# Kernel tuning notes

Hardware: AMD Instinct MI355X
Metric: run time of the kernel (lower is better)

## Reference

```python
import jax, jax.numpy as jnp
import numpy as np
from jax import lax
from jax.scipy.ndimage import map_coordinates

L = 10  # unrolled iterations (LayerNo)


def _conv(x, w, b):
    # x [N,C,H,W], w [O,I,3,3] -> 'SAME' padding == padding=1 for k=3
    y = lax.conv_general_dilated(x, w, (1, 1), 'SAME',
                                 dimension_numbers=('NCHW', 'OIHW', 'NCHW'))
    return y + b[None, :, None, None]


def _prelu(x, a):
    return jnp.where(x >= 0, x, a * x)


def _block(x, w1, b1, a1, w2, b2, a2, w3, b3):
    x = _prelu(_conv(x, w1, b1), a1)
    x = _prelu(_conv(x, w2, b2), a2)
    return _conv(x, w3, b3)


def _radon_forward(img, theta, det_count):
    # img [S,S]; parallel-beam line integrals -> [A, det_count]
    S = img.shape[0]
    c = (S - 1) / 2.0
    s = jnp.arange(det_count, dtype=img.dtype) - (det_count - 1) / 2.0
    t = jnp.arange(S, dtype=img.dtype) - (S - 1) / 2.0

    def one(a):
        ca, sa = jnp.cos(a), jnp.sin(a)
        x = s[:, None] * ca - t[None, :] * sa  # [D,S] sample cols
        y = s[:, None] * sa + t[None, :] * ca  # [D,S] sample rows
        vals = map_coordinates(img, [y + c, x + c], order=1, mode='constant', cval=0.0)
        return vals.sum(axis=1)

    return jax.vmap(one)(theta)


def _radon_backprojection(sino, theta, S):
    # sino [A,D] -> [S,S] (adjoint smear with bilinear detector interpolation)
    A, D = sino.shape
    c = (S - 1) / 2.0
    dc = (D - 1) / 2.0
    ax = jnp.arange(S, dtype=sino.dtype) - c
    Y, X = jnp.meshgrid(ax, ax, indexing='ij')  # row=y, col=x

    def one(row, a):
        ca, sa = jnp.cos(a), jnp.sin(a)
        sidx = (X * ca + Y * sa + dc).ravel()
        return map_coordinates(row, [sidx], order=1, mode='constant', cval=0.0).reshape(S, S)

    return jax.vmap(one)(sino, theta).sum(axis=0)


def _filter_sinogram(sino):
    # Ram-Lak ramp filter along detector axis with FBP normalization pi/(2*A)
    A, D = sino.shape
    n = 2048  # next power of two >= 2*D (D=729)
    F = jnp.fft.rfft(sino, n=n, axis=-1)
    ramp = (2.0 * jnp.fft.rfftfreq(n)).astype(sino.dtype)
    out = jnp.fft.irfft(F * ramp, n=n, axis=-1)[..., :D]
    return out * (jnp.pi / (2.0 * A))


def _forward(cond, x0, g, theta, theta_label,
             dw1, db1, da1, dw2, db2, da2, dw3, db3,
             pw1, pb1, pa1, pw2, pb2, pa2, pw3, pb3):
    S = x0.shape[2]
    A, D = g.shape[2], g.shape[3]
    h = jnp.zeros((1, 5, A, D), dtype=g.dtype)
    f = jnp.zeros((1, 5, S, S), dtype=g.dtype)
    for i in range(L):
        Op_f = _radon_forward(f[0, 1], theta, D)[None, None]          # [1,1,A,D]
        h = h + _block(jnp.concatenate([h, Op_f, g], axis=1),
                       dw1[i], db1[i], da1[i], dw2[i], db2[i], da2[i], dw3[i], db3[i])
        h1 = _filter_sinogram(h[0, 0])                                 # [A,D]
        OpAdj_h = _radon_backprojection(h1, theta, S)[None, None]      # [1,1,S,S]
        f = f + _block(jnp.concatenate([f, OpAdj_h], axis=1),
                       pw1[i], pb1[i], pa1[i], pw2[i], pb2[i], pa2[i], pw3[i], pb3[i])
    return (f[:, 0:1], f[:, 0:1], f[:, 0:1])


def setup_inputs() -> dict:
    key = jax.random.key(0)
    ks = jax.random.split(key, 12)
    S, A, D = 512, 60, 729

    def xavier(k, shp):
        cout, cin = shp[1], shp[2]
        std = np.sqrt(2.0 / ((cin + cout) * 9.0)).astype(np.float32)
        return jax.random.normal(k, shp, dtype=jnp.float32) * std

    ang = jnp.linspace(0.0, np.pi, A, endpoint=False).astype(jnp.float32)
    return {
        'cond': jax.random.normal(ks[0], (1, 1, S, S), dtype=jnp.float32),
        'x0': jax.random.normal(ks[1], (1, 1, S, S), dtype=jnp.float32),
        'g': jax.random.normal(ks[2], (1, 1, A, D), dtype=jnp.float32),
        'theta': ang,
        'theta_label': ang,
        'dw1': xavier(ks[3], (L, 32, 7, 3, 3)), 'db1': jnp.zeros((L, 32), jnp.float32), 'da1': 0.25 * jnp.ones((L,), jnp.float32),
        'dw2': xavier(ks[4], (L, 32, 32, 3, 3)), 'db2': jnp.zeros((L, 32), jnp.float32), 'da2': 0.25 * jnp.ones((L,), jnp.float32),
        'dw3': xavier(ks[5], (L, 5, 32, 3, 3)), 'db3': jnp.zeros((L, 5), jnp.float32),
        'pw1': xavier(ks[6], (L, 32, 6, 3, 3)), 'pb1': jnp.zeros((L, 32), jnp.float32), 'pa1': 0.25 * jnp.ones((L,), jnp.float32),
        'pw2': xavier(ks[7], (L, 32, 32, 3, 3)), 'pb2': jnp.zeros((L, 32), jnp.float32), 'pa2': 0.25 * jnp.ones((L,), jnp.float32),
        'pw3': xavier(ks[8], (L, 5, 32, 3, 3)), 'pb3': jnp.zeros((L, 5), jnp.float32),
    }


def reference(cond, x0, g, theta, theta_label,
              dw1, db1, da1, dw2, db2, da2, dw3, db3,
              pw1, pb1, pa1, pw2, pb2, pa2, pw3, pb3):
    return _forward(cond, x0, g, theta, theta_label,
                    dw1, db1, da1, dw2, db2, da2, dw3, db3,
                    pw1, pb1, pa1, pw2, pb2, pa2, pw3, pb3)
```

## Files before the change

kernel.cpp:

```cpp
#include <hip/hip_runtime.h>
#include <math.h>

#define SS 512
#define AANG 60
#define DDET 729
#define NPIX (SS*SS)
#define NSIN (AANG*DDET)
#define NTAPS 1457
#define DRS 768

typedef float v4u __attribute__((ext_vector_type(4), aligned(4)));
typedef float v4a __attribute__((ext_vector_type(4), aligned(16)));
typedef float v2u __attribute__((ext_vector_type(2), aligned(8)));
typedef float v2a __attribute__((ext_vector_type(2), aligned(4)));
typedef short short8 __attribute__((ext_vector_type(8)));
typedef short short4v __attribute__((ext_vector_type(4)));
typedef float f32x4 __attribute__((ext_vector_type(4)));

__device__ inline unsigned short f2bf(float x){
  unsigned u = __float_as_uint(x);
  return (unsigned short)((u + 0x7fffu + ((u >> 16) & 1u)) >> 16);
}

__global__ void trig_kernel(const float* __restrict__ theta, float* __restrict__ trig){
  int a = threadIdx.x;
  if (a < AANG){ trig[a] = cosf(theta[a]); trig[AANG+a] = sinf(theta[a]); }
}

__global__ void taps_kernel(float* __restrict__ taps){
  __shared__ double red[256];
  int m  = blockIdx.x;
  int mm = m - 728;
  double s = 0.0;
  for (int k = 1 + (int)threadIdx.x; k <= 1023; k += 256){
    int phase = (k*mm) & 2047;
    s += (double)k * cos((double)phase * (M_PI/1024.0));
  }
  red[threadIdx.x] = s;
  __syncthreads();
  for (int off=128; off; off>>=1){
    if ((int)threadIdx.x < off) red[threadIdx.x] += red[threadIdx.x+off];
    __syncthreads();
  }
  if (threadIdx.x==0){
    double x = (red[0]*(1.0/512.0) + ((mm & 1) ? -1.0 : 1.0)) / 2048.0;
    taps[m] = (float)(x * (M_PI/120.0));
  }
}

__global__ void transpose_all(const float* __restrict__ s2, float* __restrict__ d2,
                              const float* __restrict__ s5, float* __restrict__ d5){
  int idx = blockIdx.x*256 + (int)threadIdx.x;
  const float* src; float* dst;
  int Cout = 5, Cin = 32;
  if      (idx < 14400){              src=s2; dst=d2; }
  else if (idx < 28800){ idx-=14400;  src=s5; dst=d5; }
  else return;
  int t = idx % 9; int r = idx/9;
  int i = r % Cin; r /= Cin;
  int o = r % Cout; int l = r/Cout;
  dst[((l*Cin+i)*9+t)*Cout+o] = src[idx];
}

__global__ void transpose_w8(const float* __restrict__ src, float* __restrict__ dst, int Cin){
  int idx = blockIdx.x*256 + (int)threadIdx.x;
  int tot = 10*32*Cin*9;
  if (idx >= tot) return;
  int t = idx % 9; int r = idx/9;
  int i = r % Cin; r /= Cin;
  int o = r % 32; int l = r/32;
  int cg = o >> 3, u = o & 7;
  dst[(((l*Cin + i)*4 + cg)*9 + t)*8 + u] = src[idx];
}

__global__ void prep_bimg(const float* __restrict__ w, unsigned short* __restrict__ B){
  int idx = blockIdx.x*256 + (int)threadIdx.x;
  if (idx >= 10*9*2*64*8) return;
  int j    =  idx        & 7;
  int lane = (idx >> 3)  & 63;
  int n    = (idx >> 9)  & 1;
  int r    =  idx >> 10;
  int tap = r % 9, l = r / 9;
  int c = (lane >> 4)*8 + j;
  int o = n*16 + (lane & 15);
  float x = w[(((size_t)(l*32+o)*32 + c)*9) + tap];
  unsigned short hb = f2bf(x);
  float hf = __uint_as_float((unsigned)hb << 16);
  unsigned short lb = f2bf(x - hf);
  size_t d = (size_t)l*18432 + (size_t)tap*2048 + n*1024 + lane*8 + j;
  B[d]       = hb;
  B[d + 512] = lb;
}

__global__ void prep_bimg3(const float* __restrict__ w, unsigned short* __restrict__ B){
  int idx = blockIdx.x*256 + (int)threadIdx.x;
  if (idx >= 10*9*64*8) return;
  int j    =  idx       & 7;
  int lane = (idx >> 3) & 63;
  int r    =  idx >> 9;
  int tap = r % 9, l = r / 9;
  int c = (lane >> 4)*8 + j;
  int o = lane & 15;
  float x = (o < 5) ? w[(((size_t)(l*5+o)*32 + c)*9) + tap] : 0.f;
  unsigned short hb = f2bf(x);
  float hf = __uint_as_float((unsigned)hb << 16);
  unsigned short lb = f2bf(x - hf);
  size_t d = (size_t)l*9216 + (size_t)tap*1024 + lane*8 + j;
  B[d]       = hb;
  B[d + 512] = lb;
}

__global__ void prep_bimg1(const float* __restrict__ w, unsigned short* __restrict__ B){
  int idx = blockIdx.x*256 + (int)threadIdx.x;
  if (idx >= 10*3*2*64*8) return;
  int j    =  idx       & 7;
  int lane = (idx >> 3) & 63;
  int n    = (idx >> 9) & 1;
  int r    =  idx >> 10;
  int g = r % 3, l = r / 3;
  int t = g*4 + (lane >> 4);
  int o = n*16 + (lane & 15);
  float x = (t < 9 && j < 6) ? w[(((size_t)(l*32+o)*6 + j)*9) + t] : 0.f;
  unsigned short hb = f2bf(x);
  float hf = __uint_as_float((unsigned)hb << 16);
  unsigned short lb = f2bf(x - hf);
  size_t d = (size_t)l*6144 + (size_t)g*2048 + n*1024 + lane*8 + j;
  B[d]       = hb;
  B[d + 512] = lb;
}

__device__ inline void clipr(float al, float ial, float be, float lo, float hi,
                             float& A, float& B, bool& empty){
  if (fabsf(al) < 1e-7f){ if (be < lo || be > hi) empty = true; return; }
  float t0 = (lo - be)*ial, t1 = (hi - be)*ial;
  float mn = fminf(t0,t1), mx = fmaxf(t0,t1);
  A = fmaxf(A, mn); B = fminf(B, mx);
}

__device__ inline float samp_guard(const float* __restrict__ base, float aR, float bR,
                                   float aC, float bC, int t){
  float tp = (float)t - 255.5f;
  float R = fmaf(aR, tp, bR);
  float C = fmaf(aC, tp, bC);
  float rf = floorf(R), cf = floorf(C);
  int r0 = (int)rf, c0 = (int)cf;
  int r1 = r0+1,    c1 = c0+1;
  float fr = R - rf, fc = C - cf;
  bool r0ok = (r0>=0 && r0<SS), r1ok = (r1>=0 && r1<SS);
  bool c0ok = (c0>=0 && c0<SS), c1ok = (c1>=0 && c1<SS);
  float v00 = (r0ok && c0ok) ? base[r0*SS+c0] : 0.f;
  float v01 = (r0ok && c1ok) ? base[r0*SS+c1] : 0.f;
  float v10 = (r1ok && c0ok) ? base[r1*SS+c0] : 0.f;
  float v11 = (r1ok && c1ok) ? base[r1*SS+c1] : 0.f;
  return (1.f-fr)*((1.f-fc)*v00 + fc*v01) + fr*((1.f-fc)*v10 + fc*v11);
}

__global__ __launch_bounds__(256) void radon_fwd_kernel(
    const float* __restrict__ img, const float* __restrict__ imgT,
    const float* __restrict__ trig, float* __restrict__ out){
  int gid  = blockIdx.x*4 + ((int)threadIdx.x >> 6);
  int lane = (int)threadIdx.x & 63;
  if (gid >= NSIN) return;
  int a = gid / DDET;
  int d = gid - a*DDET;
  float ca = trig[a], sa = trig[AANG+a];
  float sd = (float)d - 364.0f;
  float Rc = fmaf(sd, sa, 255.5f);
  float Cc = fmaf(sd, ca, 255.5f);
  float aR = ca, bR = Rc, aC = -sa, bC = Cc;
  const float* base = img;
  if (fabsf(ca) > fabsf(sa)){
    base = imgT;
    float tmp;
    tmp=aR; aR=aC; aC=tmp;
    tmp=bR; bR=bC; bC=tmp;
  }
  float iaR = __builtin_amdgcn_rcpf(aR);
  float iaC = __builtin_amdgcn_rcpf(aC);
  float tiA = -255.5f, tiB = 255.5f;  bool iE=false;
  float teA = -255.5f, teB = 255.5f;  bool eE=false;
  clipr(aR,iaR,bR, 0.001f, 510.999f, tiA,tiB,iE);
  clipr(aC,iaC,bC, 0.001f, 510.999f, tiA,tiB,iE);
  clipr(aR,iaR,bR, -0.999f, 511.999f, teA,teB,eE);
  clipr(aC,iaC,bC, -0.999f, 511.999f, teA,teB,eE);
  float acc = 0.f;
  if (!eE && teA <= teB){
    int eA = max(0,   (int)floorf(teA+255.5f) - 1);
    int eB = min(511, (int)ceilf (teB+255.5f) + 1);
    int iA = (int)ceilf (tiA+255.5f) + 1;
    int iB = (int)floorf(tiB+255.5f) - 1;
    iA = max(iA, eA); iB = min(iB, eB);
    if (iE || iA > iB){
      for (int t = eA+lane; t <= eB; t += 64) acc += samp_guard(base,aR,bR,aC,bC,t);
    } else {
      for (int t = eA+lane;   t <  iA; t += 64) acc += samp_guard(base,aR,bR,aC,bC,t);
      for (int t = iB+1+lane; t <= eB; t += 64) acc += samp_guard(base,aR,bR,aC,bC,t);
      for (int t = iA+lane;   t <= iB; t += 64){
        float tp = (float)t - 255.5f;
        float R = fmaf(aR, tp, bR);
        float C = fmaf(aC, tp, bC);
        int r0 = (int)R, c0 = (int)C;
        float fr = R - (float)r0, fc = C - (float)c0;
        const float* p = base + r0*SS + c0;
        float v00 = p[0], v01 = p[1], v10 = p[SS], v11 = p[SS+1];
        float top = v00 + fc*(v01-v00);
        float bot = v10 + fc*(v11-v10);
        acc += top + fr*(bot-top);
      }
    }
  }
  for (int off=32; off; off>>=1) acc += __shfl_down(acc, off);
  if (lane==0) out[gid] = acc;
}

__global__ __launch_bounds__(256) void filter_kernel2(
    const float* __restrict__ h0, const float* __restrict__ taps,
    float* __restrict__ h1){
  __shared__ float red[256];
  int a  = blockIdx.x / 12;
  int jb = blockIdx.x - a*12;
  int jl = (int)threadIdx.x & 63;
  int kq = (int)threadIdx.x >> 6;
  int j  = jb*64 + jl;
  float acc = 0.f;
  if (j < DDET){
    const float* row = h0 + a*DDET;
    const float* tp  = taps + 728 + j;
    int k0 = kq*183;
    int k1 = min(k0+183, DDET);
    for (int k=k0;k<k1;k++) acc = fmaf(row[k], tp[-k], acc);
  }
  red[threadIdx.x] = acc;
  __syncthreads();
  if ((int)threadIdx.x < 64 && j < DDET){
    float s = red[jl] + red[64+jl] + red[128+jl] + red[192+jl];
    h1[a*DDET + j] = s;
  }
}

__global__ __launch_bounds__(256) void backproj_kernel(
    const float* __restrict__ h1, const float* __restrict__ trig,
    unsigned short* __restrict__ hi8, unsigned short* __restrict__ lo8){
  __shared__ float sh[AANG*28];
  __shared__ int   sbase[AANG];
  __shared__ float strig[2*AANG];
  int tid = threadIdx.x;
  int x0 = (blockIdx.x & 31) * 16, y0 = (blockIdx.x >> 5) * 16;
  if (tid < 2*AANG) strig[tid] = trig[tid];
  __syncthreads();
  if (tid < AANG){
    float ca = strig[tid], sa = strig[AANG+tid];
    float Xa = (float)x0 - 255.5f, Xb = Xa + 15.f;
    float Ya = (float)y0 - 255.5f, Yb = Ya + 15.f;
    float s00 = Xa*ca + Ya*sa, s01 = Xb*ca + Ya*sa;
    float s10 = Xa*ca + Yb*sa, s11 = Xb*ca + Yb*sa;
    float mn = fminf(fminf(s00,s01), fminf(s10,s11)) + 364.0f;
    sbase[tid] = (int)floorf(mn) - 2;
  }
  __syncthreads();
  for (int s = tid; s < AANG*28; s += 256){
    int a = s / 28, j = s - a*28;
    int idx = sbase[a] + j;
    sh[s] = (idx >= 0 && idx < DDET) ? h1[a*DDET + idx] : 0.f;
  }
  __syncthreads();
  int x = x0 + (tid & 15), y = y0 + (tid >> 4);
  float X = (float)x - 255.5f, Y = (float)y - 255.5f;
  float acc = 0.f;
  #pragma unroll 6
  for (int a=0;a<AANG;a++){
    float sidx = fmaf(X, strig[a], fmaf(Y, strig[AANG+a], 364.0f));
    float ff = floorf(sidx);
    int k = (int)ff - sbase[a];
    float fi = sidx - ff;
    float v0 = sh[a*28+k], v1 = sh[a*28+k+1];
    acc += v0 + fi*(v1-v0);
  }
  unsigned short hb = f2bf(acc);
  float hf = __uint_as_float((unsigned)hb << 16);
  unsigned short lb = f2bf(acc - hf);
  size_t p8 = ((size_t)(y*SS + x))*8 + 5;
  hi8[p8] = hb;
  lo8[p8] = lb;
}

__global__ __launch_bounds__(256) void conv3x3_dual1(
    const float* __restrict__ in1, int Cin1,
    const float* __restrict__ in2, int Cin2,
    const float* __restrict__ wt,
    const float* __restrict__ bias, const float* __restrict__ prelu,
    unsigned short* __restrict__ outHi, unsigned short* __restrict__ outLo)
{
  const int W = DDET, HW = NSIN;
  int pix = blockIdx.x*256 + (int)threadIdx.x;
  if (pix >= NSIN) return;
  int cg = blockIdx.y;
  int y = pix / W, x = pix - y*W;
  bool ym = y>0, yp = y<AANG-1, xm = x>0, xp = x<W-1;
  float acc[8];
  #pragma unroll
  for (int o=0;o<8;o++) acc[o] = bias[cg*8+o];
  const float* wch = wt + cg*72;
  for (int part=0; part<2; part++){
    const float* src = part ? in2 : in1;
    int nch = part ? Cin2 : Cin1;
    const float* ip = src + pix;
    for (int i=0;i<nch;i++, ip+=HW, wch+=288){
      float p4 = ip[0];
      float p0=0,p1=0,p2=0,p3=0,p5=0,p6=0,p7=0,p8=0;
      if (ym){ p1 = ip[-W]; if (xm) p0 = ip[-W-1]; if (xp) p2 = ip[-W+1]; }
      if (xm) p3 = ip[-1];
      if (xp) p5 = ip[1];
      if (yp){ p7 = ip[W]; if (xm) p6 = ip[W-1]; if (xp) p8 = ip[W+1]; }
      float p[9] = {p0,p1,p2,p3,p4,p5,p6,p7,p8};
      #pragma unroll
      for (int t=0;t<9;t++){
        float v = p[t];
        #pragma unroll
        for (int o=0;o<8;o++) acc[o] = fmaf(v, wch[t*8+o], acc[o]);
      }
    }
  }
  float aa = *prelu;
  short8 vh, vl;
  #pragma unroll
  for (int o=0;o<8;o++){
    float s = acc[o];
    s = (s>=0.f) ? s : aa*s;
    unsigned short hb = f2bf(s);
    float hf = __uint_as_float((unsigned)hb << 16);
    unsigned short lb = f2bf(s - hf);
    vh[o] = (short)hb; vl[o] = (short)lb;
  }
  size_t base = ((size_t)(y+1)*DRS + x)*32 + cg*8;
  *(short8*)(outHi + base) = vh;
  *(short8*)(outLo + base) = vl;
}

__global__ __launch_bounds__(64) void dual_mfma32(
    const unsigned short* __restrict__ hiB, const unsigned short* __restrict__ loB,
    const unsigned short* __restrict__ Bimg,
    const float* __restrict__ bias, const float* __restrict__ prelu,
    float* __restrict__ out)
{
  int y  = blockIdx.y;
  int lane = (int)threadIdx.x;
  int xw = blockIdx.x*64;
  int lm = lane & 15, lq = lane >> 4;
  int laneoff = lm*32 + lq*8;
  f32x4 acc[4][2];
  #pragma unroll
  for (int s=0;s<4;s++){ acc[s][0] = (f32x4)0.f; acc[s][1] = (f32x4)0.f; }
  const short8* Bf = (const short8*)Bimg;
  #pragma unroll
  for (int dy=-1; dy<=1; dy++){
    const unsigned short* rh = hiB + (size_t)(y+dy+1)*DRS*32;
    const unsigned short* rl = loB + (size_t)(y+dy+1)*DRS*32;
    #pragma unroll
    for (int dx=-1; dx<=1; dx++){
      int tap = (dy+1)*3 + (dx+1);
      const short8* bp8 = Bf + tap*256 + lane;
      short8 bh0 = bp8[0];
      short8 bl0 = bp8[64];
      short8 bh1 = bp8[128];
      short8 bl1 = bp8[192];
      int xoff = (xw + dx)*32 + laneoff;
      #pragma unroll
      for (int s=0; s<4; s++){
        short8 ah = *(const short8*)(rh + xoff + s*512);
        short8 al = *(const short8*)(rl + xoff + s*512);
        acc[s][0] = __builtin_amdgcn_mfma_f32_16x16x32_bf16(ah, bh0, acc[s][0], 0,0,0);
        acc[s][1] = __builtin_amdgcn_mfma_f32_16x16x32_bf16(ah, bh1, acc[s][1], 0,0,0);
        acc[s][0] = __builtin_amdgcn_mfma_f32_16x16x32_bf16(al, bh0, acc[s][0], 0,0,0);
        acc[s][1] = __builtin_amdgcn_mfma_f32_16x16x32_bf16(al, bh1, acc[s][1], 0,0,0);
        acc[s][0] = __builtin_amdgcn_mfma_f32_16x16x32_bf16(ah, bl0, acc[s][0], 0,0,0);
        acc[s][1] = __builtin_amdgcn_mfma_f32_16x16x32_bf16(ah, bl1, acc[s][1], 0,0,0);
      }
    }
  }
  float aa = *prelu;
  #pragma unroll
  for (int s=0;s<4;s++){
    int px0 = xw + s*16 + lq*4;
    #pragma unroll
    for (int n=0;n<2;n++){
      int o = n*16 + lm;
      float bv = bias[o];
      f32x4 v = acc[s][n];
      v.x+=bv; v.y+=bv; v.z+=bv; v.w+=bv;
      v.x=(v.x>=0.f)?v.x:aa*v.x; v.y=(v.y>=0.f)?v.y:aa*v.y;
      v.z=(v.z>=0.f)?v.z:aa*v.z; v.w=(v.w>=0.f)?v.w:aa*v.w;
      float* op = out + (size_t)o*NSIN + y*DDET + px0;
      if (px0 + 3 <= DDET-1){
        v4u st; st.x=v.x; st.y=v.y; st.z=v.z; st.w=v.w;
        *(v4u*)op = st;
      } else {
        if (px0   <= DDET-1) op[0] = v.x;
        if (px0+1 <= DDET-1) op[1] = v.y;
        if (px0+2 <= DDET-1) op[2] = v.z;
      }
    }
  }
}

template<int COUT, int W>
__global__ __launch_bounds__(256) void conv3x3_fast2(
    const float* __restrict__ in1, int Cin1,
    const float* __restrict__ wt,
    const float* __restrict__ bias,
    float* __restrict__ out, int H)
{
  __shared__ float red[128*COUT];
  int HW = H*W;
  int pl = (int)threadIdx.x & 127;
  int half = (int)threadIdx.x >> 7;
  int pix = blockIdx.x*128 + pl;
  bool valid = (pix < HW);
  float acc[COUT];
  #pragma unroll
  for (int o=0;o<COUT;o++) acc[o] = 0.f;
  if (valid){
    int y = pix / W, x = pix - y*W;
    bool ym = y>0, yp = y<H-1, xm = x>0, xp = x<W-1;
    int nch = Cin1 >> 1;
    const float* wr = wt + half*nch*9*COUT;
    const float* ip = in1 + pix + (size_t)half*nch*HW;
    for (int i=0;i<nch;i++, ip+=HW){
      float p4 = ip[0];
      float p0=0,p1=0,p2=0,p3=0,p5=0,p6=0,p7=0,p8=0;
      if (ym){ p1 = ip[-W]; if (xm) p0 = ip[-W-1]; if (xp) p2 = ip[-W+1]; }
      if (xm) p3 = ip[-1];
      if (xp) p5 = ip[1];
      if (yp){ p7 = ip[W]; if (xm) p6 = ip[W-1]; if (xp) p8 = ip[W+1]; }
      float p[9] = {p0,p1,p2,p3,p4,p5,p6,p7,p8};
      #pragma unroll
      for (int t=0;t<9;t++){
        float v = p[t];
        #pragma unroll
        for (int o=0;o<COUT;o++) acc[o] = fmaf(v, wr[t*COUT+o], acc[o]);
      }
      wr += 9*COUT;
    }
  }
  if (half == 1){
    #pragma unroll
    for (int o=0;o<COUT;o++) red[pl*COUT+o] = acc[o];
  }
  __syncthreads();
  if (half == 0 && valid){
    float* op = out + pix;
    #pragma unroll
    for (int o=0;o<COUT;o++)
      op[o*HW] += acc[o] + red[pl*COUT+o] + bias[o];
  }
}

__global__ __launch_bounds__(256) void prim1_mfma(
    const unsigned short* __restrict__ hi8, const unsigned short* __restrict__ lo8,
    const unsigned short* __restrict__ Bimg1,
    const float* __restrict__ bias, const float* __restrict__ prelu,
    unsigned short* __restrict__ outHi, unsigned short* __restrict__ outLo)
{
  __shared__ unsigned int tr[4][64][33];
  int b = blockIdx.x;
  int by = b >> 1, half = b & 1;
  int y = ((by & 7) << 6) | (by >> 3);
  int wv = (int)threadIdx.x >> 6;
  int lane = (int)threadIdx.x & 63;
  int xw = half*256 + wv*64;
  int lm = lane & 15, lq = lane >> 4;
  f32x4 acc[4][2];
  #pragma unroll
  for (int s=0;s<4;s++){ acc[s][0] = (f32x4)0.f; acc[s][1] = (f32x4)0.f; }
  bool fast = (y>0) && (y<511) && (xw!=0) && (xw!=448);
  const short8* Bf = (const short8*)Bimg1;
  #pragma unroll
  for (int g=0; g<3; g++){
    const short8* bp8 = Bf + g*256 + lane;
    short8 bh0 = bp8[0];
    short8 bl0 = bp8[64];
    short8 bh1 = bp8[128];
    short8 bl1 = bp8[192];
    int t = g*4 + lq; if (t > 8) t = 8;
    int dy = (t >= 6) ? 1 : ((t >= 3) ? 0 : -1);
    int dx = t - (dy+1)*3 - 1;
    int row = y + dy;
    #pragma unroll
    for (int s=0; s<4; s++){
      short8 ah, al;
      int px = xw + s*16 + lm + dx;
      if (fast){
        size_t off = ((size_t)row*SS + px)*8;
        ah = *(const short8*)(hi8 + off);
        al = *(const short8*)(lo8 + off);
      } else {
        bool ok = ((unsigned)row < 512u) && ((unsigned)px < 512u);
        size_t off = ok ? ((size_t)row*SS + px)*8 : 0;
        ah = ok ? *(const short8*)(hi8 + off) : (short8)0;
        al = ok ? *(const short8*)(lo8 + off) : (short8)0;
      }
      acc[s][0] = __builtin_amdgcn_mfma_f32_16x16x32_bf16(ah, bh0, acc[s][0], 0,0,0);
      acc[s][1] = __builtin_amdgcn_mfma_f32_16x16x32_bf16(ah, bh1, acc[s][1], 0,0,0);
      acc[s][0] = __builtin_amdgcn_mfma_f32_16x16x32_bf16(al, bh0, acc[s][0], 0,0,0);
      acc[s][1] = __builtin_amdgcn_mfma_f32_16x16x32_bf16(al, bh1, acc[s][1], 0,0,0);
      acc[s][0] = __builtin_amdgcn_mfma_f32_16x16x32_bf16(ah, bl0, acc[s][0], 0,0,0);
      acc[s][1] = __builtin_amdgcn_mfma_f32_16x16x32_bf16(ah, bl1, acc[s][1], 0,0,0);
    }
  }
  float aa = *prelu;
  #pragma unroll
  for (int s=0;s<4;s++){
    #pragma unroll
    for (int n=0;n<2;n++){
      int o = n*16 + lm;
      float bv = bias[o];
      f32x4 v = acc[s][n];
      v.x+=bv; v.y+=bv; v.z+=bv; v.w+=bv;
      v.x=(v.x>=0.f)?v.x:aa*v.x; v.y=(v.y>=0.f)?v.y:aa*v.y;
      v.z=(v.z>=0.f)?v.z:aa*v.z; v.w=(v.w>=0.f)?v.w:aa*v.w;
      #pragma unroll
      for (int r=0;r<4;r++){
        float x = v[r];
        unsigned short hb = f2bf(x);
        float hf = __uint_as_float((unsigned)hb << 16);
        unsigned short lb = f2bf(x - hf);
        tr[wv][s*16 + lq*4 + r][o] = ((unsigned)hb << 16) | (unsigned)lb;
      }
    }
  }
  __syncthreads();
  int c8 = lane & 3;
  int pxl = lane >> 2;
  #pragma unroll
  for (int k=0;k<4;k++){
    int px = pxl + k*16;
    short8 vh, vl;
    #pragma unroll
    for (int j=0;j<8;j++){
      unsigned p = tr[wv][px][c8*8 + j];
      vh[j] = (short)(p >> 16);
      vl[j] = (short)(p & 0xffffu);
    }
    size_t base = ((size_t)(y*SS + xw + px))*32 + c8*8;
    *(short8*)(outHi + base) = vh;
    *(short8*)(outLo + base) = vl;
  }
}

__global__ __launch_bounds__(256) void conv_mfma32(
    const unsigned short* __restrict__ hiB, const unsigned short* __restrict__ loB,
    const unsigned short* __restrict__ Bimg,
    const float* __restrict__ bias, const float* __restrict__ prelu,
    unsigned short* __restrict__ outHi, unsigned short* __restrict__ outLo)
{
  __shared__ unsigned int tr[4][64][33];
  int b = blockIdx.x;
  int by = b >> 1, half = b & 1;
  int y = ((by & 7) << 6) | (by >> 3);
  int wv = (int)threadIdx.x >> 6;
  int lane = (int)threadIdx.x & 63;
  int xw = half*256 + wv*64;
  int lm = lane & 15, lq = lane >> 4;
  int laneoff = lm*32 + lq*8;
  f32x4 acc[4][2];
  #pragma unroll
  for (int s=0;s<4;s++){ acc[s][0] = (f32x4)0.f; acc[s][1] = (f32x4)0.f; }
  bool fastx = (xw != 0) && (xw != 448);
  const short8* Bf = (const short8*)Bimg;
  #pragma unroll
  for (int dy=-1; dy<=1; dy++){
    int yy = y + dy;
    if ((unsigned)yy >= 512u) continue;
    const unsigned short* rh = hiB + (size_t)yy*512*32;
    const unsigned short* rl = loB + (size_t)yy*512*32;
    #pragma unroll
    for (int dx=-1; dx<=1; dx++){
      int tap = (dy+1)*3 + (dx+1);
      const short8* bp8 = Bf + tap*256 + lane;
      short8 bh0 = bp8[0];
      short8 bl0 = bp8[64];
      short8 bh1 = bp8[128];
      short8 bl1 = bp8[192];
      int xoff = (xw + dx)*32 + laneoff;
      #pragma unroll
      for (int s=0; s<4; s++){
        short8 ah, al;
        const unsigned short* ph = rh + xoff + s*512;
        const unsigned short* pl = rl + xoff + s*512;
        if (fastx){
          ah = *(const short8*)ph;
          al = *(const short8*)pl;
        } else {
          int x = xw + s*16 + lm + dx;
          bool ok = ((unsigned)x < 512u);
          ah = ok ? *(const short8*)ph : (short8)0;
          al = ok ? *(const short8*)pl : (short8)0;
        }
        acc[s][0] = __builtin_amdgcn_mfma_f32_16x16x32_bf16(ah, bh0, acc[s][0], 0,0,0);
        acc[s][1] = __builtin_amdgcn_mfma_f32_16x16x32_bf16(ah, bh1, acc[s][1], 0,0,0);
        acc[s][0] = __builtin_amdgcn_mfma_f32_16x16x32_bf16(al, bh0, acc[s][0], 0,0,0);
        acc[s][1] = __builtin_amdgcn_mfma_f32_16x16x32_bf16(al, bh1, acc[s][1], 0,0,0);
        acc[s][0] = __builtin_amdgcn_mfma_f32_16x16x32_bf16(ah, bl0, acc[s][0], 0,0,0);
        acc[s][1] = __builtin_amdgcn_mfma_f32_16x16x32_bf16(ah, bl1, acc[s][1], 0,0,0);
      }
    }
  }
  float aa = *prelu;
  #pragma unroll
  for (int s=0;s<4;s++){
    #pragma unroll
    for (int n=0;n<2;n++){
      int o = n*16 + lm;
      float bv = bias[o];
      f32x4 v = acc[s][n];
      v.x+=bv; v.y+=bv; v.z+=bv; v.w+=bv;
      v.x=(v.x>=0.f)?v.x:aa*v.x; v.y=(v.y>=0.f)?v.y:aa*v.y;
      v.z=(v.z>=0.f)?v.z:aa*v.z; v.w=(v.w>=0.f)?v.w:aa*v.w;
      #pragma unroll
      for (int r=0;r<4;r++){
        float x = v[r];
        unsigned short hb = f2bf(x);
        float hf = __uint_as_float((unsigned)hb << 16);
        unsigned short lb = f2bf(x - hf);
        tr[wv][s*16 + lq*4 + r][o] = ((unsigned)hb << 16) | (unsigned)lb;
      }
    }
  }
  __syncthreads();
  int c8 = lane & 3;
  int pxl = lane >> 2;
  #pragma unroll
  for (int k=0;k<4;k++){
    int px = pxl + k*16;
    short8 vh, vl;
    #pragma unroll
    for (int j=0;j<8;j++){
      unsigned p = tr[wv][px][c8*8 + j];
      vh[j] = (short)(p >> 16);
      vl[j] = (short)(p & 0xffffu);
    }
    size_t base = ((size_t)(y*SS + xw + px))*32 + c8*8;
    *(short8*)(outHi + base) = vh;
    *(short8*)(outLo + base) = vl;
  }
}

__global__ __launch_bounds__(256) void duo_mfma(
    const unsigned short* __restrict__ hiB, const unsigned short* __restrict__ loB,
    const unsigned short* __restrict__ Bimg3,
    const float* __restrict__ bias,
    float* __restrict__ f,
    float* __restrict__ fout, float* __restrict__ tout,
    unsigned short* __restrict__ hi8, unsigned short* __restrict__ lo8)
{
  __shared__ unsigned int t8[4][64][6];
  int b = blockIdx.x;
  int by = b >> 1, half = b & 1;
  int y = ((by & 7) << 6) | (by >> 3);
  int wv = (int)threadIdx.x >> 6;
  int lane = (int)threadIdx.x & 63;
  int xw = half*256 + wv*64;
  int lm = lane & 15, lq = lane >> 4;
  int laneoff = lm*32 + lq*8;
  f32x4 acc[4];
  #pragma unroll
  for (int s=0;s<4;s++) acc[s] = (f32x4)0.f;
  bool fastx = (xw != 0) && (xw != 448);
  const short8* Bf = (const short8*)Bimg3;
  #pragma unroll
  for (int dy=-1; dy<=1; dy++){
    int yy = y + dy;
    if ((unsigned)yy >= 512u) continue;
    const unsigned short* rh = hiB + (size_t)yy*512*32;
    const unsigned short* rl = loB + (size_t)yy*512*32;
    #pragma unroll
    for (int dx=-1; dx<=1; dx++){
      int tap = (dy+1)*3 + (dx+1);
      const short8* bp8 = Bf + tap*128 + lane;
      short8 bh = bp8[0];
      short8 bl = bp8[64];
      int xoff = (xw + dx)*32 + laneoff;
      #pragma unroll
      for (int s=0; s<4; s++){
        short8 ah, al;
        const unsigned short* ph = rh + xoff + s*512;
        const unsigned short* pl = rl + xoff + s*512;
        if (fastx){
          ah = *(const short8*)ph;
          al = *(const short8*)pl;
        } else {
          int x = xw + s*16 + lm + dx;
          bool ok = ((unsigned)x < 512u);
          ah = ok ? *(const short8*)ph : (short8)0;
          al = ok ? *(const short8*)pl : (short8)0;
        }
        acc[s] = __builtin_amdgcn_mfma_f32_16x16x32_bf16(ah, bh, acc[s], 0,0,0);
        acc[s] = __builtin_amdgcn_mfma_f32_16x16x32_bf16(al, bh, acc[s], 0,0,0);
        acc[s] = __builtin_amdgcn_mfma_f32_16x16x32_bf16(ah, bl, acc[s], 0,0,0);
      }
    }
  }
  if (lm < 5){
    float bv = bias[lm];
    #pragma unroll
    for (int s=0;s<4;s++){
      int px0 = xw + s*16 + lq*4;
      float* op = f + (size_t)lm*NPIX + y*SS + px0;
      f32x4 old = *(const f32x4*)op;
      f32x4 v = acc[s];
      v.x += old.x + bv; v.y += old.y + bv;
      v.z += old.z + bv; v.w += old.w + bv;
      *(f32x4*)op = v;
      #pragma unroll
      for (int r=0;r<4;r++){
        float x = v[r];
        unsigned short hb = f2bf(x);
        float hf = __uint_as_float((unsigned)hb << 16);
        unsigned short lb = f2bf(x - hf);
        t8[wv][s*16 + lq*4 + r][lm] = ((unsigned)hb << 16) | (unsigned)lb;
      }
      if (lm == 1){
        tout[(px0  )*SS + y] = v.x;
        tout[(px0+1)*SS + y] = v.y;
        tout[(px0+2)*SS + y] = v.z;
        tout[(px0+3)*SS + y] = v.w;
      }
      if (lm == 0 && fout){
        float* q = fout + y*SS + px0;
        *(f32x4*)q = v;
        *(f32x4*)(q + NPIX) = v;
        *(f32x4*)(q + 2*NPIX) = v;
      }
    }
  }
  __syncthreads();
  {
    unsigned c0 = t8[wv][lane][0], c1 = t8[wv][lane][1], c2 = t8[wv][lane][2];
    unsigned c3 = t8[wv][lane][3], c4 = t8[wv][lane][4];
    size_t base = ((size_t)(y*SS + xw + lane))*8;
    short4v vh; vh[0]=(short)(c0>>16); vh[1]=(short)(c1>>16); vh[2]=(short)(c2>>16); vh[3]=(short)(c3>>16);
    short4v vl; vl[0]=(short)(c0&0xffffu); vl[1]=(short)(c1&0xffffu); vl[2]=(short)(c2&0xffffu); vl[3]=(short)(c3&0xffffu);
    *(short4v*)(hi8 + base) = vh;
    *(short4v*)(lo8 + base) = vl;
    hi8[base+4] = (unsigned short)(c4>>16);
    lo8[base+4] = (unsigned short)(c4&0xffffu);
  }
}

extern "C" void kernel_launch(void* const* d_in, const int* in_sizes, int n_in,
                              void* d_out, int out_size, void* d_ws, size_t ws_size,
                              hipStream_t stream){
  const float* g     = (const float*)d_in[2];
  const float* theta = (const float*)d_in[3];
  const float* dw1 = (const float*)d_in[5];
  const float* db1 = (const float*)d_in[6];
  const float* da1 = (const float*)d_in[7];
  const float* dw2 = (const float*)d_in[8];
  const float* db2 = (const float*)d_in[9];
  const float* da2 = (const float*)d_in[10];
  const float* dw3 = (const float*)d_in[11];
  const float* db3 = (const float*)d_in[12];
  const float* pw1 = (const float*)d_in[13];
  const float* pb1 = (const float*)d_in[14];
  const float* pa1 = (const float*)d_in[15];
  const float* pw2 = (const float*)d_in[16];
  const float* pb2 = (const float*)d_in[17];
  const float* pa2 = (const float*)d_in[18];
  const float* pw3 = (const float*)d_in[19];
  const float* pb3 = (const float*)d_in[20];

  float* ws     = (float*)d_ws;
  float* trig   = ws;
  float* taps   = ws + 128;
  float* h      = ws + 2048;
  float* opf    = h + 5*NSIN;
  float* gcopy  = opf + NSIN;
  float* h1     = gcopy + NSIN;
  float* f      = h1 + NSIN;
  float* bp     = f + 5*NPIX;
  float* imgT   = bp + NPIX;
  float* dualT1 = imgT + NPIX;
  float* dualT2 = dualT1 + 32*NSIN;
  float* primT2slot = dualT2 + 32*NSIN;
  unsigned short* primHi = (unsigned short*)primT2slot;
  unsigned short* primLo = primHi + (size_t)32*NPIX;
  unsigned short* nhwcHi = (unsigned short*)(primT2slot + 32*NPIX);
  unsigned short* nhwcLo = nhwcHi + (size_t)32*NPIX;
  float* wsp   = (float*)(nhwcLo + (size_t)32*NPIX);
  float* wtd3  = wsp;
  float* wtp3  = wsp + 14400;
  float* wtd1b = wsp + 28800;
  float* wtd2b = wsp + 48960;
  float* wtp1b = wsp + 141120;
  unsigned short* Bimg  = (unsigned short*)(wsp + 158400);
  unsigned short* Bimg2 = Bimg + 184320;
  unsigned short* Bimg3 = Bimg2 + 184320;
  unsigned short* Bimg1 = Bimg3 + 92160;
  const size_t DUALSZ = (size_t)64 + (size_t)62*DRS*32 + 64;
  unsigned short* dualHiRaw = Bimg1 + 61440;
  unsigned short* dualLoRaw = dualHiRaw + DUALSZ;
  unsigned short* dualHi = dualHiRaw + 64;
  unsigned short* dualLo = dualLoRaw + 64;
  unsigned short* nh8Hi = dualLoRaw + DUALSZ;
  unsigned short* nh8Lo = nh8Hi + (size_t)NPIX*8;

  hipMemsetAsync(h, 0, (size_t)(5*NSIN)*sizeof(float), stream);
  hipMemsetAsync(f, 0, (size_t)(7*NPIX)*sizeof(float), stream);
  hipMemsetAsync(dualHiRaw, 0, 2*DUALSZ*sizeof(unsigned short), stream);
  hipMemsetAsync(nh8Hi, 0, (size_t)2*NPIX*8*sizeof(unsigned short), stream);
  hipMemcpyAsync(gcopy, g, (size_t)NSIN*sizeof(float), hipMemcpyDeviceToDevice, stream);
  trig_kernel<<<1,64,0,stream>>>(theta, trig);
  taps_kernel<<<NTAPS,256,0,stream>>>(taps);
  transpose_all<<<(28800+255)/256,256,0,stream>>>(dw3,wtd3, pw3,wtp3);
  transpose_w8<<<(20160+255)/256,256,0,stream>>>(dw1, wtd1b, 7);
  prep_bimg<<<(92160+255)/256,256,0,stream>>>(pw2, Bimg);
  prep_bimg<<<(92160+255)/256,256,0,stream>>>(dw2, Bimg2);
  prep_bimg3<<<(46080+255)/256,256,0,stream>>>(pw3, Bimg3);
  prep_bimg1<<<(30720+255)/256,256,0,stream>>>(pw1, Bimg1);

  const int GD = (NSIN+255)/256;

  for (int i=0;i<10;i++){
    radon_fwd_kernel<<<(NSIN+3)/4,256,0,stream>>>(f + NPIX, imgT, trig, opf);
    conv3x3_dual1<<<dim3(GD,4),256,0,stream>>>(h, 5, opf, 2, wtd1b+(size_t)i*7*288,
                                               db1+(size_t)i*32, da1+i, dualHi, dualLo);
    dual_mfma32<<<dim3(12,AANG),64,0,stream>>>(dualHi, dualLo, Bimg2+(size_t)i*18432,
                                               db2+(size_t)i*32, da2+i, dualT2);
    conv3x3_fast2<5,DDET><<<(NSIN+127)/128,256,0,stream>>>(dualT2, 32, wtd3+i*1440, db3+(size_t)i*5, h, AANG);
    filter_kernel2<<<AANG*12,256,0,stream>>>(h, taps, h1);
    backproj_kernel<<<NPIX/256,256,0,stream>>>(h1, trig, nh8Hi, nh8Lo);
    prim1_mfma<<<1024,256,0,stream>>>(nh8Hi, nh8Lo, Bimg1+(size_t)i*6144,
                                      pb1+(size_t)i*32, pa1+i, nhwcHi, nhwcLo);
    conv_mfma32<<<1024,256,0,stream>>>(nhwcHi, nhwcLo, Bimg+(size_t)i*18432, pb2+(size_t)i*32, pa2+i, primHi, primLo);
    duo_mfma<<<1024,256,0,stream>>>(primHi, primLo, Bimg3+(size_t)i*9216, pb3+(size_t)i*5, f,
                                    (i==9) ? (float*)d_out : nullptr, imgT, nh8Hi, nh8Lo);
  }
}
```

Measured before the change: 1.882 ms.

## Replace scalar dual first conv with split-bf16 MFMA over padded NHWC8 sinogram

The first dual-branch 3x3 conv (7 input channels: h, the forward projection and g) moves from a scalar FMA kernel to an MFMA kernel using hi/lo bf16 splitting. To feed it, the radon forward kernel, the third dual conv and a one-time g conversion now write their outputs directly into a padded 8-channel NHWC bf16 hi/lo buffer. This replaces the planar fp32 reads and scalar inner loop with matrix-core work and an LDS transpose for the output. The cost is extra scattered 2-byte stores in the producer kernels and a small precision loss from the three-term bf16 split.

```diff
diff --git a/kernel.cpp b/kernel.cpp
--- a/kernel.cpp
+++ b/kernel.cpp
@@ -60,17 +60,6 @@
   int i = r % Cin; r /= Cin;
   int o = r % Cout; int l = r/Cout;
   dst[((l*Cin+i)*9+t)*Cout+o] = src[idx];
-}
-
-__global__ void transpose_w8(const float* __restrict__ src, float* __restrict__ dst, int Cin){
-  int idx = blockIdx.x*256 + (int)threadIdx.x;
-  int tot = 10*32*Cin*9;
-  if (idx >= tot) return;
-  int t = idx % 9; int r = idx/9;
-  int i = r % Cin; r /= Cin;
-  int o = r % 32; int l = r/32;
-  int cg = o >> 3, u = o & 7;
-  dst[(((l*Cin + i)*4 + cg)*9 + t)*8 + u] = src[idx];
 }
 
 __global__ void prep_bimg(const float* __restrict__ w, unsigned short* __restrict__ B){
@@ -110,7 +99,7 @@
   B[d + 512] = lb;
 }
 
-__global__ void prep_bimg1(const float* __restrict__ w, unsigned short* __restrict__ B){
+__global__ void prep_bimg1c(const float* __restrict__ w, unsigned short* __restrict__ B, int Cin){
   int idx = blockIdx.x*256 + (int)threadIdx.x;
   if (idx >= 10*3*2*64*8) return;
   int j    =  idx       & 7;
@@ -120,13 +109,27 @@
   int g = r % 3, l = r / 3;
   int t = g*4 + (lane >> 4);
   int o = n*16 + (lane & 15);
-  float x = (t < 9 && j < 6) ? w[(((size_t)(l*32+o)*6 + j)*9) + t] : 0.f;
+  float x = (t < 9 && j < Cin) ? w[(((size_t)(l*32+o)*Cin + j)*9) + t] : 0.f;
   unsigned short hb = f2bf(x);
   float hf = __uint_as_float((unsigned)hb << 16);
   unsigned short lb = f2bf(x - hf);
   size_t d = (size_t)l*6144 + (size_t)g*2048 + n*1024 + lane*8 + j;
   B[d]       = hb;
   B[d + 512] = lb;
+}
+
+__global__ void g_to_nhwc8(const float* __restrict__ g,
+                           unsigned short* __restrict__ s8hi, unsigned short* __restrict__ s8lo){
+  int idx = blockIdx.x*256 + (int)threadIdx.x;
+  if (idx >= NSIN) return;
+  int a = idx / DDET, d = idx - a*DDET;
+  float x = g[idx];
+  unsigned short hb = f2bf(x);
+  float hf = __uint_as_float((unsigned)hb << 16);
+  unsigned short lb = f2bf(x - hf);
+  size_t p8 = ((size_t)(a+1)*DRS + d)*8 + 6;
+  s8hi[p8] = hb;
+  s8lo[p8] = lb;
 }
 
 __device__ inline void clipr(float al, float ial, float be, float lo, float hi,
@@ -157,7 +160,8 @@
 
 __global__ __launch_bounds__(256) void radon_fwd_kernel(
     const float* __restrict__ img, const float* __restrict__ imgT,
-    const float* __restrict__ trig, float* __restrict__ out){
+    const float* __restrict__ trig,
+    unsigned short* __restrict__ s8hi, unsigned short* __restrict__ s8lo){
   int gid  = blockIdx.x*4 + ((int)threadIdx.x >> 6);
   int lane = (int)threadIdx.x & 63;
   if (gid >= NSIN) return;
@@ -210,7 +214,14 @@
     }
   }
   for (int off=32; off; off>>=1) acc += __shfl_down(acc, off);
-  if (lane==0) out[gid] = acc;
+  if (lane==0){
+    unsigned short hb = f2bf(acc);
+    float hf = __uint_as_float((unsigned)hb << 16);
+    unsigned short lb = f2bf(acc - hf);
+    size_t p8 = ((size_t)(a+1)*DRS + d)*8 + 5;
+    s8hi[p8] = hb;
+    s8lo[p8] = lb;
+  }
 }
 
 __global__ __launch_bounds__(256) void filter_kernel2(
@@ -284,57 +295,86 @@
   lo8[p8] = lb;
 }
 
-__global__ __launch_bounds__(256) void conv3x3_dual1(
-    const float* __restrict__ in1, int Cin1,
-    const float* __restrict__ in2, int Cin2,
-    const float* __restrict__ wt,
+__global__ __launch_bounds__(64) void dual1_mfma(
+    const unsigned short* __restrict__ hi8, const unsigned short* __restrict__ lo8,
+    const unsigned short* __restrict__ Bimg1d,
     const float* __restrict__ bias, const float* __restrict__ prelu,
     unsigned short* __restrict__ outHi, unsigned short* __restrict__ outLo)
 {
-  const int W = DDET, HW = NSIN;
-  int pix = blockIdx.x*256 + (int)threadIdx.x;
-  if (pix >= NSIN) return;
-  int cg = blockIdx.y;
-  int y = pix / W, x = pix - y*W;
-  bool ym = y>0, yp = y<AANG-1, xm = x>0, xp = x<W-1;
-  float acc[8];
-  #pragma unroll
-  for (int o=0;o<8;o++) acc[o] = bias[cg*8+o];
-  const float* wch = wt + cg*72;
-  for (int part=0; part<2; part++){
-    const float* src = part ? in2 : in1;
-    int nch = part ? Cin2 : Cin1;
-    const float* ip = src + pix;
-    for (int i=0;i<nch;i++, ip+=HW, wch+=288){
-      float p4 = ip[0];
-      float p0=0,p1=0,p2=0,p3=0,p5=0,p6=0,p7=0,p8=0;
-      if (ym){ p1 = ip[-W]; if (xm) p0 = ip[-W-1]; if (xp) p2 = ip[-W+1]; }
-      if (xm) p3 = ip[-1];
-      if (xp) p5 = ip[1];
-      if (yp){ p7 = ip[W]; if (xm) p6 = ip[W-1]; if (xp) p8 = ip[W+1]; }
-      float p[9] = {p0,p1,p2,p3,p4,p5,p6,p7,p8};
+  __shared__ unsigned int tr[64][33];
+  int y  = blockIdx.y;
+  int lane = (int)threadIdx.x;
+  int xw = blockIdx.x*64;
+  int lm = lane & 15, lq = lane >> 4;
+  f32x4 acc[4][2];
+  #pragma unroll
+  for (int s=0;s<4;s++){ acc[s][0] = (f32x4)0.f; acc[s][1] = (f32x4)0.f; }
+  const short8* Bf = (const short8*)Bimg1d;
+  #pragma unroll
+  for (int g=0; g<3; g++){
+    const short8* bp8 = Bf + g*256 + lane;
+    short8 bh0 = bp8[0];
+    short8 bl0 = bp8[64];
+    short8 bh1 = bp8[128];
+    short8 bl1 = bp8[192];
+    int t = g*4 + lq; if (t > 8) t = 8;
+    int dy = (t >= 6) ? 1 : ((t >= 3) ? 0 : -1);
+    int dx = t - (dy+1)*3 - 1;
+    int row = y + dy + 1;
+    #pragma unroll
+    for (int s=0; s<4; s++){
+      int px = xw + s*16 + lm + dx;
+      size_t off = (size_t)(row*DRS + px)*8;
+      short8 ah = *(const short8*)(hi8 + off);
+      short8 al = *(const short8*)(lo8 + off);
+      acc[s][0] = __builtin_amdgcn_mfma_f32_16x16x32_bf16(ah, bh0, acc[s][0], 0,0,0);
+      acc[s][1] = __builtin_amdgcn_mfma_f32_16x16x32_bf16(ah, bh1, acc[s][1], 0,0,0);
+      acc[s][0] = __builtin_amdgcn_mfma_f32_16x16x32_bf16(al, bh0, acc[s][0], 0,0,0);
+      acc[s][1] = __builtin_amdgcn_mfma_f32_16x16x32_bf16(al, bh1, acc[s][1], 0,0,0);
+      acc[s][0] = __builtin_amdgcn_mfma_f32_16x16x32_bf16(ah, bl0, acc[s][0], 0,0,0);
+      acc[s][1] = __builtin_amdgcn_mfma_f32_16x16x32_bf16(ah, bl1, acc[s][1], 0,0,0);
+    }
+  }
+  float aa = *prelu;
+  #pragma unroll
+  for (int s=0;s<4;s++){
+    #pragma unroll
+    for (int n=0;n<2;n++){
+      int o = n*16 + lm;
+      float bv = bias[o];
+      f32x4 v = acc[s][n];
+      v.x+=bv; v.y+=bv; v.z+=bv; v.w+=bv;
+      v.x=(v.x>=0.f)?v.x:aa*v.x; v.y=(v.y>=0.f)?v.y:aa*v.y;
+      v.z=(v.z>=0.f)?v.z:aa*v.z; v.w=(v.w>=0.f)?v.w:aa*v.w;
       #pragma unroll
-      for (int t=0;t<9;t++){
-        float v = p[t];
-        #pragma unroll
-        for (int o=0;o<8;o++) acc[o] = fmaf(v, wch[t*8+o], acc[o]);
-      }
-    }
-  }
-  float aa = *prelu;
-  short8 vh, vl;
-  #pragma unroll
-  for (int o=0;o<8;o++){
-    float s = acc[o];
-    s = (s>=0.f) ? s : aa*s;
-    unsigned short hb = f2bf(s);
-    float hf = __uint_as_float((unsigned)hb << 16);
-    unsigned short lb = f2bf(s - hf);
-    vh[o] = (short)hb; vl[o] = (short)lb;
-  }
-  size_t base = ((size_t)(y+1)*DRS + x)*32 + cg*8;
-  *(short8*)(outHi + base) = vh;
-  *(short8*)(outLo + base) = vl;
+      for (int r=0;r<4;r++){
+        float x = v[r];
+        unsigned short hb = f2bf(x);
+        float hf = __uint_as_float((unsigned)hb << 16);
+        unsigned short lb = f2bf(x - hf);
+        tr[s*16 + lq*4 + r][o] = ((unsigned)hb << 16) | (unsigned)lb;
+      }
+    }
+  }
+  __syncthreads();
+  int c8 = lane & 3;
+  int pxl = lane >> 2;
+  #pragma unroll
+  for (int k=0;k<4;k++){
+    int px = pxl + k*16;
+    int x = xw + px;
+    if (x > 728) continue;
+    short8 vh, vl;
+    #pragma unroll
+    for (int j=0;j<8;j++){
+      unsigned p = tr[px][c8*8 + j];
+      vh[j] = (short)(p >> 16);
+      vl[j] = (short)(p & 0xffffu);
+    }
+    size_t base = ((size_t)(y+1)*DRS + x)*32 + c8*8;
+    *(short8*)(outHi + base) = vh;
+    *(short8*)(outLo + base) = vl;
+  }
 }
 
 __global__ __launch_bounds__(64) void dual_mfma32(
@@ -408,7 +448,8 @@
     const float* __restrict__ in1, int Cin1,
     const float* __restrict__ wt,
     const float* __restrict__ bias,
-    float* __restrict__ out, int H)
+    float* __restrict__ out, int H,
+    unsigned short* __restrict__ s8hi, unsigned short* __restrict__ s8lo)
 {
   __shared__ float red[128*COUT];
   int HW = H*W;
@@ -448,10 +489,19 @@
   }
   __syncthreads();
   if (half == 0 && valid){
+    int y = pix / W, x = pix - y*W;
     float* op = out + pix;
-    #pragma unroll
-    for (int o=0;o<COUT;o++)
-      op[o*HW] += acc[o] + red[pl*COUT+o] + bias[o];
+    size_t p8 = ((size_t)(y+1)*DRS + x)*8;
+    #pragma unroll
+    for (int o=0;o<COUT;o++){
+      float nv = op[o*HW] + acc[o] + red[pl*COUT+o] + bias[o];
+      op[o*HW] = nv;
+      unsigned short hb = f2bf(nv);
+      float hf = __uint_as_float((unsigned)hb << 16);
+      unsigned short lb = f2bf(nv - hf);
+      s8hi[p8+o] = hb;
+      s8lo[p8+o] = lb;
+    }
   }
 }
 
@@ -796,37 +846,43 @@
   unsigned short* Bimg2 = Bimg + 184320;
   unsigned short* Bimg3 = Bimg2 + 184320;
   unsigned short* Bimg1 = Bimg3 + 92160;
+  unsigned short* Bimg1d = Bimg1 + 61440;
   const size_t DUALSZ = (size_t)64 + (size_t)62*DRS*32 + 64;
-  unsigned short* dualHiRaw = Bimg1 + 61440;
+  unsigned short* dualHiRaw = Bimg1d + 61440;
   unsigned short* dualLoRaw = dualHiRaw + DUALSZ;
   unsigned short* dualHi = dualHiRaw + 64;
   unsigned short* dualLo = dualLoRaw + 64;
   unsigned short* nh8Hi = dualLoRaw + DUALSZ;
   unsigned short* nh8Lo = nh8Hi + (size_t)NPIX*8;
+  const size_t S8SZ = (size_t)64 + (size_t)62*DRS*8 + 64;
+  unsigned short* s8HiRaw = nh8Lo + (size_t)NPIX*8;
+  unsigned short* s8LoRaw = s8HiRaw + S8SZ;
+  unsigned short* s8Hi = s8HiRaw + 64;
+  unsigned short* s8Lo = s8LoRaw + 64;
 
   hipMemsetAsync(h, 0, (size_t)(5*NSIN)*sizeof(float), stream);
   hipMemsetAsync(f, 0, (size_t)(7*NPIX)*sizeof(float), stream);
   hipMemsetAsync(dualHiRaw, 0, 2*DUALSZ*sizeof(unsigned short), stream);
   hipMemsetAsync(nh8Hi, 0, (size_t)2*NPIX*8*sizeof(unsigned short), stream);
-  hipMemcpyAsync(gcopy, g, (size_t)NSIN*sizeof(float), hipMemcpyDeviceToDevice, stream);
+  hipMemsetAsync(s8HiRaw, 0, 2*S8SZ*sizeof(unsigned short), stream);
   trig_kernel<<<1,64,0,stream>>>(theta, trig);
   taps_kernel<<<NTAPS,256,0,stream>>>(taps);
   transpose_all<<<(28800+255)/256,256,0,stream>>>(dw3,wtd3, pw3,wtp3);
-  transpose_w8<<<(20160+255)/256,256,0,stream>>>(dw1, wtd1b, 7);
   prep_bimg<<<(92160+255)/256,256,0,stream>>>(pw2, Bimg);
   prep_bimg<<<(92160+255)/256,256,0,stream>>>(dw2, Bimg2);
   prep_bimg3<<<(46080+255)/256,256,0,stream>>>(pw3, Bimg3);
-  prep_bimg1<<<(30720+255)/256,256,0,stream>>>(pw1, Bimg1);
-
-  const int GD = (NSIN+255)/256;
+  prep_bimg1c<<<(30720+255)/256,256,0,stream>>>(pw1, Bimg1, 6);
+  prep_bimg1c<<<(30720+255)/256,256,0,stream>>>(dw1, Bimg1d, 7);
+  g_to_nhwc8<<<(NSIN+255)/256,256,0,stream>>>(g, s8Hi, s8Lo);
 
   for (int i=0;i<10;i++){
-    radon_fwd_kernel<<<(NSIN+3)/4,256,0,stream>>>(f + NPIX, imgT, trig, opf);
-    conv3x3_dual1<<<dim3(GD,4),256,0,stream>>>(h, 5, opf, 2, wtd1b+(size_t)i*7*288,
-                                               db1+(size_t)i*32, da1+i, dualHi, dualLo);
+    radon_fwd_kernel<<<(NSIN+3)/4,256,0,stream>>>(f + NPIX, imgT, trig, s8Hi, s8Lo);
+    dual1_mfma<<<dim3(12,AANG),64,0,stream>>>(s8Hi, s8Lo, Bimg1d+(size_t)i*6144,
+                                              db1+(size_t)i*32, da1+i, dualHi, dualLo);
     dual_mfma32<<<dim3(12,AANG),64,0,stream>>>(dualHi, dualLo, Bimg2+(size_t)i*18432,
                                                db2+(size_t)i*32, da2+i, dualT2);
-    conv3x3_fast2<5,DDET><<<(NSIN+127)/128,256,0,stream>>>(dualT2, 32, wtd3+i*1440, db3+(size_t)i*5, h, AANG);
+    conv3x3_fast2<5,DDET><<<(NSIN+127)/128,256,0,stream>>>(dualT2, 32, wtd3+i*1440, db3+(size_t)i*5,
+                                                           h, AANG, s8Hi, s8Lo);
     filter_kernel2<<<AANG*12,256,0,stream>>>(h, taps, h1);
     backproj_kernel<<<NPIX/256,256,0,stream>>>(h1, trig, nh8Hi, nh8Lo);
     prim1_mfma<<<1024,256,0,stream>>>(nh8Hi, nh8Lo, Bimg1+(size_t)i*6144,
```

Result: no change. 1.850 ms (-1.7%).
